# Optimization experiments

Measured on AMD Instinct MI355X. Metric: run time of the kernel, lower is better.

## Reference

```python
import jax, jax.numpy as jnp
import numpy as np

ALPHA = 0.2  # tf.nn.leaky_relu default

def leaky(x):
    return jnp.where(x >= 0, x, ALPHA * x)

def segment_softmax(score, seg, num_segments):
    m = jax.ops.segment_max(score, seg, num_segments=num_segments)
    e = jnp.exp(score - m[seg])
    denom = jax.ops.segment_sum(e, seg, num_segments=num_segments)
    return e / denom[seg]

def setup_inputs() -> dict:
    key = jax.random.key(0)
    ks = jax.random.split(key, 8)
    E, NE, NR, D, U = 500000, 100000, 1000, 128, 128
    return {
        "h_index": jax.random.randint(ks[0], (E,), 0, NE),
        "r_index": jax.random.randint(ks[1], (E,), 0, NR),
        "t_index": jax.random.randint(ks[2], (E,), 0, NE),
        "entity_embeddings": jax.random.normal(ks[3], (NE, D), jnp.float32),
        "relation_embeddings": jax.random.normal(ks[4], (NR, D), jnp.float32),
        "W": jax.random.normal(ks[5], (3 * D, U), jnp.float32) * 0.05,
        "a": jax.random.normal(ks[6], (U, 1), jnp.float32) * 0.1,
        "a_b": jnp.zeros((1,), jnp.float32),
        "bias": jnp.zeros((U,), jnp.float32),
    }

def reference(h_index, r_index, t_index, entity_embeddings, relation_embeddings, W, a, a_b, bias):
    num_entities = entity_embeddings.shape[0]
    h = entity_embeddings[h_index]          # [E, D]
    r = relation_embeddings[r_index]        # [E, D]
    t = entity_embeddings[t_index]          # [E, D]
    feats = jnp.concatenate([h, r, t], axis=-1) @ W  # [E, U]
    # att_kernel Dense(1, activation=leaky_relu), then wrapped again in att_activation
    score = leaky(leaky(feats @ a + a_b))[:, 0]      # [E]
    alpha = segment_softmax(score, h_index, num_entities)
    msg = feats * alpha[:, None]                     # gcn_mapper: edge features * weight
    reduced = jax.ops.segment_sum(msg, h_index, num_segments=num_entities)  # [NE, U]
    out = reduced + bias                             # identity_updater returns reduced_msg
    return jax.nn.relu(out)
```

## Files before the change

kernel.cpp:

```cpp
#include <hip/hip_runtime.h>
#include <hip/hip_bf16.h>

#define ALPHA2 0.04f

typedef __attribute__((ext_vector_type(8))) short short8;
typedef __attribute__((ext_vector_type(4))) float floatx4;
typedef __attribute__((ext_vector_type(8))) unsigned short ushort8;

__device__ __forceinline__ unsigned short f2bf(float f) {
    unsigned u = __float_as_uint(f);
    unsigned r = (u + 0x7fffu + ((u >> 16) & 1u)) >> 16;
    return (unsigned short)r;
}
__device__ __forceinline__ float bf2f(unsigned short h) {
    return __uint_as_float((unsigned)h << 16);
}

__device__ __forceinline__ void async_copy16(const float* g, float* lds_base) {
    __builtin_amdgcn_global_load_lds(
        (const __attribute__((address_space(1))) unsigned int*)g,
        (__attribute__((address_space(3))) unsigned int*)lds_base, 16, 0, 0);
}


__global__ void k_prep(const float* __restrict__ W, unsigned short* __restrict__ Bfr,
                       int* __restrict__ count, int NE) {
    int idx = blockIdx.x * blockDim.x + threadIdx.x;
    if (idx < 3 * 128 * 128) {
        int kk = idx & 7, n = (idx >> 3) & 127, g = idx >> 10;
        int slice = g >> 4, kc = (g >> 2) & 3, quad = g & 3;
        int k = kc * 32 + quad * 8 + kk;
        Bfr[idx] = f2bf(W[(size_t)(slice * 128 + k) * 128 + n]);
    }
    if (idx < NE) count[idx] = 0;
}

__global__ __launch_bounds__(256, 4) void k_gemm_all(
        const float* __restrict__ ent, const float* __restrict__ rel,
        const unsigned short* __restrict__ Bfr,
        unsigned short* __restrict__ Pb, unsigned short* __restrict__ Qb,
        unsigned short* __restrict__ Rb,
        float* __restrict__ s1, float* __restrict__ s3, float* __restrict__ s2,
        const float* __restrict__ avec, int NE, int NR, int NBent, int NBrel,
        const int* __restrict__ hidx, int* __restrict__ count,
        int* __restrict__ rank, int E) {
    __shared__ __align__(16) float Ash[64 * 128];
    int tid = threadIdx.x;
    int b = blockIdx.x;
    int ngemm = NBent + NBrel;

    if (b >= ngemm) {
        int e = (b - ngemm) * 256 + tid;
        if (e < E) rank[e] = atomicAdd(count + hidx[e], 1);
        return;
    }

    bool isEnt = b < NBent;
    const float* In = isEnt ? ent : rel;
    int nrows = isEnt ? NE : NR;
    int rowbase = (isEnt ? b : b - NBent) * 64;

    int wave = tid >> 6, lane = tid & 63;

    #pragma unroll
    for (int i = 0; i < 8; ++i) {
        int r = wave * 16 + i * 2 + (lane >> 5);
        int grow = rowbase + r;
        if (grow > nrows - 1) grow = nrows - 1;
        int c = (lane & 31) ^ (r & 7);
        async_copy16(In + (size_t)grow * 128 + c * 4,
                     Ash + (size_t)(wave * 16 + i * 2) * 128);
    }
    __syncthreads();

    int m16 = lane & 15, quad = lane >> 4;
    int rs = wave * 16;
    int R = rs + m16, sw = R & 7;
    const float4* rowp = (const float4*)(Ash + (size_t)R * 128);

    float av[8];
    #pragma unroll
    for (int j = 0; j < 8; ++j) av[j] = avec[j * 16 + m16];

    int nphase = isEnt ? 2 : 1;
    for (int ph = 0; ph < nphase; ++ph) {
        int slice; unsigned short* Out; float* svec;
        if (isEnt) { slice = ph ? 2 : 0; Out = ph ? Qb : Pb; svec = ph ? s3 : s1; }
        else       { slice = 1; Out = Rb; svec = s2; }

        floatx4 acc[8];
        #pragma unroll
        for (int j = 0; j < 8; ++j) acc[j] = (floatx4){0.f, 0.f, 0.f, 0.f};

        short8 bf0[8], bf1[8];
        auto loadB = [&](int kc, short8* dst) {
            const unsigned short* bb =
                Bfr + (size_t)((slice * 4 + kc) * 4 + quad) * 1024 + m16 * 8;
            #pragma unroll
            for (int j = 0; j < 8; ++j) dst[j] = *(const short8*)(bb + j * 128);
        };
        auto doMfma = [&](int kc, short8* bf) {
            int c0 = kc * 8 + quad * 2;
            float4 fa = rowp[c0 ^ sw];
            float4 fb = rowp[(c0 + 1) ^ sw];
            short8 af;
            af[0] = (short)f2bf(fa.x); af[1] = (short)f2bf(fa.y);
            af[2] = (short)f2bf(fa.z); af[3] = (short)f2bf(fa.w);
            af[4] = (short)f2bf(fb.x); af[5] = (short)f2bf(fb.y);
            af[6] = (short)f2bf(fb.z); af[7] = (short)f2bf(fb.w);
            #pragma unroll
            for (int j = 0; j < 8; ++j)
                acc[j] = __builtin_amdgcn_mfma_f32_16x16x32_bf16(af, bf[j], acc[j], 0, 0, 0);
        };
        loadB(0, bf0);
        loadB(1, bf1);
        doMfma(0, bf0);
        loadB(2, bf0);
        doMfma(1, bf1);
        loadB(3, bf1);
        doMfma(2, bf0);
        doMfma(3, bf1);

        #pragma unroll
        for (int reg = 0; reg < 4; ++reg) {
            int row = rowbase + rs + quad * 4 + reg;
            float part = 0.f;
            ushort8 v;
            #pragma unroll
            for (int j = 0; j < 8; ++j) {
                float x = acc[j][reg];
                part = fmaf(x, av[j], part);
                v[j] = f2bf(x);
            }
            #pragma unroll
            for (int off = 1; off < 16; off <<= 1) part += __shfl_xor(part, off);
            if (row < nrows) {
                *(ushort8*)(Out + (size_t)row * 128 + m16 * 8) = v;
                if (m16 == 0) svec[row] = part;
            }
        }
    }
}

__device__ __forceinline__ int block_incl_scan256(int s, int* sh, int t) {
    sh[t] = s; __syncthreads();
    #pragma unroll
    for (int off = 1; off < 256; off <<= 1) {
        int x = 0;
        if (t >= off) x = sh[t - off];
        __syncthreads();
        sh[t] += x;
        __syncthreads();
    }
    return sh[t];
}

__global__ __launch_bounds__(256) void k_scan_a(const int* __restrict__ count, int NE,
                                                int* __restrict__ bsum) {
    __shared__ int sh[256];
    int b = blockIdx.x, t = threadIdx.x;
    int base = b * 1024 + t * 4, s = 0;
    #pragma unroll
    for (int j = 0; j < 4; ++j) { int i = base + j; if (i < NE) s += count[i]; }
    sh[t] = s; __syncthreads();
    for (int off = 128; off > 0; off >>= 1) {
        if (t < off) sh[t] += sh[t + off];
        __syncthreads();
    }
    if (t == 0) bsum[b] = sh[0];
}

__global__ __launch_bounds__(256) void k_scan_c(const int* __restrict__ count, int NE,
                                                const int* __restrict__ bsum, int NB,
                                                int* __restrict__ rowstart, int E) {
    __shared__ int sh[256];
    int b = blockIdx.x, t = threadIdx.x;
    int sb = (t < NB) ? bsum[t] : 0;
    (void)block_incl_scan256(sb, sh, t);
    int base0 = (b == 0) ? 0 : sh[b - 1];
    __syncthreads();
    int base = b * 1024 + t * 4;
    int v[4]; int s = 0;
    #pragma unroll
    for (int j = 0; j < 4; ++j) { int i = base + j; v[j] = (i < NE) ? count[i] : 0; s += v[j]; }
    int incl = block_incl_scan256(s, sh, t);
    int excl = base0 + incl - s;
    #pragma unroll
    for (int j = 0; j < 4; ++j) {
        int i = base + j;
        if (i < NE) { rowstart[i] = excl; excl += v[j]; }
    }
    if (b == 0 && t == 0) rowstart[NE] = E;
}

__global__ void k_score_scatter(const int* __restrict__ h, const int* __restrict__ r,
                                const int* __restrict__ t, const float* __restrict__ s1,
                                const float* __restrict__ s2, const float* __restrict__ s3,
                                const float* __restrict__ a_b,
                                const int* __restrict__ rowstart, const int* __restrict__ rank,
                                uint2* __restrict__ rt_s, int E) {
    int e = blockIdx.x * blockDim.x + threadIdx.x;
    if (e >= E) return;
    int hi = h[e], ri = r[e], ti = t[e];
    float x = s1[hi] + s2[ri] + s3[ti] + a_b[0];
    float sc = (x >= 0.f) ? x : ALPHA2 * x;
    float ev = __expf(sc);
    rt_s[rowstart[hi] + rank[e]] = make_uint2(((unsigned)ri << 17) | (unsigned)ti,
                                              __float_as_uint(ev));
}

__global__ __launch_bounds__(256) void k_aggregate(const int* __restrict__ rowstart,
                                                   const uint2* __restrict__ rt_s,
                                                   const unsigned short* __restrict__ Pb,
                                                   const unsigned short* __restrict__ Qb,
                                                   const unsigned short* __restrict__ Rb,
                                                   const float* __restrict__ bias,
                                                   float* __restrict__ out, int NE) {
    int gid = blockIdx.x * blockDim.x + threadIdx.x;
    int n = gid >> 4;
    int sl = gid & 15;
    if (n >= NE) return;
    int start = rowstart[n], end = rowstart[n + 1];
    int c0 = sl * 8;
    float acc[8] = {};
    float evsum = 0.f;
    int i = start;
    for (; i + 4 <= end; i += 4) {
        uint2 m0 = rt_s[i], m1 = rt_s[i + 1], m2 = rt_s[i + 2], m3 = rt_s[i + 3];
        float ev0 = __uint_as_float(m0.y), ev1 = __uint_as_float(m1.y);
        float ev2 = __uint_as_float(m2.y), ev3 = __uint_as_float(m3.y);
        ushort8 q0 = *(const ushort8*)(Qb + (size_t)(m0.x & 0x1FFFFu) * 128 + c0);
        ushort8 rr0 = *(const ushort8*)(Rb + (size_t)(m0.x >> 17) * 128 + c0);
        ushort8 q1 = *(const ushort8*)(Qb + (size_t)(m1.x & 0x1FFFFu) * 128 + c0);
        ushort8 rr1 = *(const ushort8*)(Rb + (size_t)(m1.x >> 17) * 128 + c0);
        ushort8 q2 = *(const ushort8*)(Qb + (size_t)(m2.x & 0x1FFFFu) * 128 + c0);
        ushort8 rr2 = *(const ushort8*)(Rb + (size_t)(m2.x >> 17) * 128 + c0);
        ushort8 q3 = *(const ushort8*)(Qb + (size_t)(m3.x & 0x1FFFFu) * 128 + c0);
        ushort8 rr3 = *(const ushort8*)(Rb + (size_t)(m3.x >> 17) * 128 + c0);
        evsum += (ev0 + ev1) + (ev2 + ev3);
        #pragma unroll
        for (int j = 0; j < 8; ++j) {
            acc[j] = fmaf(ev0, bf2f(q0[j]) + bf2f(rr0[j]), acc[j]);
            acc[j] = fmaf(ev1, bf2f(q1[j]) + bf2f(rr1[j]), acc[j]);
            acc[j] = fmaf(ev2, bf2f(q2[j]) + bf2f(rr2[j]), acc[j]);
            acc[j] = fmaf(ev3, bf2f(q3[j]) + bf2f(rr3[j]), acc[j]);
        }
    }
    for (; i < end; ++i) {
        uint2 m0 = rt_s[i];
        float ev0 = __uint_as_float(m0.y);
        ushort8 q0 = *(const ushort8*)(Qb + (size_t)(m0.x & 0x1FFFFu) * 128 + c0);
        ushort8 rr0 = *(const ushort8*)(Rb + (size_t)(m0.x >> 17) * 128 + c0);
        evsum += ev0;
        #pragma unroll
        for (int j = 0; j < 8; ++j)
            acc[j] = fmaf(ev0, bf2f(q0[j]) + bf2f(rr0[j]), acc[j]);
    }
    float bi[8];
    #pragma unroll
    for (int j = 0; j < 8; ++j) bi[j] = bias[j * 16 + sl];
    float o[8];
    if (end > start) {
        float inv = 1.f / evsum;
        ushort8 pb = *(const ushort8*)(Pb + (size_t)n * 128 + c0);
        #pragma unroll
        for (int j = 0; j < 8; ++j) o[j] = bf2f(pb[j]) + acc[j] * inv + bi[j];
    } else {
        #pragma unroll
        for (int j = 0; j < 8; ++j) o[j] = bi[j];
    }
    #pragma unroll
    for (int j = 0; j < 8; ++j)
        out[(size_t)n * 128 + j * 16 + sl] = fmaxf(o[j], 0.f);
}

static inline size_t align_up(size_t x, size_t a) { return (x + a - 1) / a * a; }

extern "C" void kernel_launch(void* const* d_in, const int* in_sizes, int n_in,
                              void* d_out, int out_size, void* d_ws, size_t ws_size,
                              hipStream_t stream) {
    const int* h_index = (const int*)d_in[0];
    const int* r_index = (const int*)d_in[1];
    const int* t_index = (const int*)d_in[2];
    const float* ent = (const float*)d_in[3];
    const float* rel = (const float*)d_in[4];
    const float* W = (const float*)d_in[5];
    const float* a = (const float*)d_in[6];
    const float* a_b = (const float*)d_in[7];
    const float* bias = (const float*)d_in[8];
    float* out = (float*)d_out;

    int E = in_sizes[0];
    int NE = in_sizes[3] / 128;
    int NR = in_sizes[4] / 128;

    char* p = (char*)d_ws;
    auto alloc = [&](size_t bytes) { char* q = p; p += align_up(bytes, 256); return (void*)q; };
    unsigned short* Pb = (unsigned short*)alloc((size_t)NE * 128 * 2);
    unsigned short* Qb = (unsigned short*)alloc((size_t)NE * 128 * 2);
    unsigned short* Rb = (unsigned short*)alloc((size_t)NR * 128 * 2);
    unsigned short* Bfr = (unsigned short*)alloc((size_t)3 * 128 * 128 * 2);
    float* s1 = (float*)alloc((size_t)NE * 4);
    float* s3 = (float*)alloc((size_t)NE * 4);
    float* s2 = (float*)alloc((size_t)NR * 4);
    int* count = (int*)alloc((size_t)NE * 4);
    int* rowstart = (int*)alloc((size_t)(NE + 1) * 4);
    int* rank = (int*)alloc((size_t)E * 4);
    int NB = (NE + 1023) / 1024;
    int* bsum = (int*)alloc((size_t)NB * 4);
    uint2* rt_s = (uint2*)alloc((size_t)E * 8);
    (void)ws_size; (void)n_in; (void)out_size;

    int nprep = (NE > 3 * 128 * 128) ? NE : 3 * 128 * 128;
    k_prep<<<(nprep + 255) / 256, 256, 0, stream>>>(W, Bfr, count, NE);
    int NBent = (NE + 63) / 64, NBrel = (NR + 63) / 64;
    int NBcnt = (E + 255) / 256;
    k_gemm_all<<<NBent + NBrel + NBcnt, 256, 0, stream>>>(
        ent, rel, Bfr, Pb, Qb, Rb, s1, s3, s2, a, NE, NR, NBent, NBrel,
        h_index, count, rank, E);
    k_scan_a<<<NB, 256, 0, stream>>>(count, NE, bsum);
    k_scan_c<<<NB, 256, 0, stream>>>(count, NE, bsum, NB, rowstart, E);
    k_score_scatter<<<(E + 255) / 256, 256, 0, stream>>>(h_index, r_index, t_index,
                                                         s1, s2, s3, a_b, rowstart,
                                                         rank, rt_s, E);
    k_aggregate<<<(NE * 16 + 255) / 256, 256, 0, stream>>>(rowstart, rt_s, Pb, Qb, Rb,
                                                           bias, out, NE);
}
```

Measured before the change: 200.3 us.

## Fuse scan, score scatter and aggregation into one cooperative persistent kernel

Replaces the four post-GEMM launches (two scan passes, score scatter, aggregate) with a single cooperative kernel that uses grid-wide syncs between phases and grid-stride loops over edges and nodes. The aim is to remove kernel launch gaps and tail effects between small dependent kernels. It adds grid.sync costs, caps the grid at resident occupancy, and keeps the old multi-kernel path as a fallback if the cooperative launch fails.

```diff
diff --git a/kernel.cpp b/kernel.cpp
--- a/kernel.cpp
+++ b/kernel.cpp
@@ -1,5 +1,8 @@
 #include <hip/hip_runtime.h>
 #include <hip/hip_bf16.h>
+#include <hip/hip_cooperative_groups.h>
+
+namespace cg = cooperative_groups;
 
 #define ALPHA2 0.04f
 
@@ -155,71 +158,25 @@
     return sh[t];
 }
 
-__global__ __launch_bounds__(256) void k_scan_a(const int* __restrict__ count, int NE,
-                                                int* __restrict__ bsum) {
-    __shared__ int sh[256];
-    int b = blockIdx.x, t = threadIdx.x;
-    int base = b * 1024 + t * 4, s = 0;
-    #pragma unroll
-    for (int j = 0; j < 4; ++j) { int i = base + j; if (i < NE) s += count[i]; }
-    sh[t] = s; __syncthreads();
-    for (int off = 128; off > 0; off >>= 1) {
-        if (t < off) sh[t] += sh[t + off];
-        __syncthreads();
-    }
-    if (t == 0) bsum[b] = sh[0];
-}
-
-__global__ __launch_bounds__(256) void k_scan_c(const int* __restrict__ count, int NE,
-                                                const int* __restrict__ bsum, int NB,
-                                                int* __restrict__ rowstart, int E) {
-    __shared__ int sh[256];
-    int b = blockIdx.x, t = threadIdx.x;
-    int sb = (t < NB) ? bsum[t] : 0;
-    (void)block_incl_scan256(sb, sh, t);
-    int base0 = (b == 0) ? 0 : sh[b - 1];
-    __syncthreads();
-    int base = b * 1024 + t * 4;
-    int v[4]; int s = 0;
-    #pragma unroll
-    for (int j = 0; j < 4; ++j) { int i = base + j; v[j] = (i < NE) ? count[i] : 0; s += v[j]; }
-    int incl = block_incl_scan256(s, sh, t);
-    int excl = base0 + incl - s;
-    #pragma unroll
-    for (int j = 0; j < 4; ++j) {
-        int i = base + j;
-        if (i < NE) { rowstart[i] = excl; excl += v[j]; }
-    }
-    if (b == 0 && t == 0) rowstart[NE] = E;
-}
-
-__global__ void k_score_scatter(const int* __restrict__ h, const int* __restrict__ r,
-                                const int* __restrict__ t, const float* __restrict__ s1,
-                                const float* __restrict__ s2, const float* __restrict__ s3,
-                                const float* __restrict__ a_b,
-                                const int* __restrict__ rowstart, const int* __restrict__ rank,
-                                uint2* __restrict__ rt_s, int E) {
-    int e = blockIdx.x * blockDim.x + threadIdx.x;
-    if (e >= E) return;
+__device__ __forceinline__ void scatter_one(int e,
+        const int* __restrict__ h, const int* __restrict__ r, const int* __restrict__ t,
+        const float* __restrict__ s1, const float* __restrict__ s2,
+        const float* __restrict__ s3, float ab0,
+        const int* __restrict__ rowstart, const int* __restrict__ rank,
+        uint2* __restrict__ rt_s) {
     int hi = h[e], ri = r[e], ti = t[e];
-    float x = s1[hi] + s2[ri] + s3[ti] + a_b[0];
+    float x = s1[hi] + s2[ri] + s3[ti] + ab0;
     float sc = (x >= 0.f) ? x : ALPHA2 * x;
     float ev = __expf(sc);
     rt_s[rowstart[hi] + rank[e]] = make_uint2(((unsigned)ri << 17) | (unsigned)ti,
                                               __float_as_uint(ev));
 }
 
-__global__ __launch_bounds__(256) void k_aggregate(const int* __restrict__ rowstart,
-                                                   const uint2* __restrict__ rt_s,
-                                                   const unsigned short* __restrict__ Pb,
-                                                   const unsigned short* __restrict__ Qb,
-                                                   const unsigned short* __restrict__ Rb,
-                                                   const float* __restrict__ bias,
-                                                   float* __restrict__ out, int NE) {
-    int gid = blockIdx.x * blockDim.x + threadIdx.x;
-    int n = gid >> 4;
-    int sl = gid & 15;
-    if (n >= NE) return;
+__device__ __forceinline__ void agg_one(int n, int sl,
+        const int* __restrict__ rowstart, const uint2* __restrict__ rt_s,
+        const unsigned short* __restrict__ Pb, const unsigned short* __restrict__ Qb,
+        const unsigned short* __restrict__ Rb,
+        const float* __restrict__ bias, float* __restrict__ out) {
     int start = rowstart[n], end = rowstart[n + 1];
     int c0 = sl * 8;
     float acc[8] = {};
@@ -274,6 +231,123 @@
         out[(size_t)n * 128 + j * 16 + sl] = fmaxf(o[j], 0.f);
 }
 
+__global__ __launch_bounds__(256, 4) void k_post(
+        const int* __restrict__ count, int NE, int NB98,
+        int* __restrict__ bsum, int* __restrict__ rowstart, int E,
+        const int* __restrict__ h, const int* __restrict__ r, const int* __restrict__ t,
+        const float* __restrict__ s1, const float* __restrict__ s2,
+        const float* __restrict__ s3, const float* __restrict__ a_b,
+        const int* __restrict__ rank, uint2* __restrict__ rt_s,
+        const unsigned short* __restrict__ Pb, const unsigned short* __restrict__ Qb,
+        const unsigned short* __restrict__ Rb,
+        const float* __restrict__ bias, float* __restrict__ out) {
+    cg::grid_group grid = cg::this_grid();
+    __shared__ int sh[256];
+    int b = blockIdx.x, tx = threadIdx.x, nb = gridDim.x;
+
+    if (b < NB98) {
+        int base = b * 1024 + tx * 4, s = 0;
+        #pragma unroll
+        for (int j = 0; j < 4; ++j) { int i = base + j; if (i < NE) s += count[i]; }
+        sh[tx] = s; __syncthreads();
+        for (int off = 128; off > 0; off >>= 1) {
+            if (tx < off) sh[tx] += sh[tx + off];
+            __syncthreads();
+        }
+        if (tx == 0) bsum[b] = sh[0];
+    }
+    grid.sync();
+
+    if (b < NB98) {
+        int sb = (tx < NB98) ? bsum[tx] : 0;
+        (void)block_incl_scan256(sb, sh, tx);
+        int base0 = (b == 0) ? 0 : sh[b - 1];
+        __syncthreads();
+        int base = b * 1024 + tx * 4;
+        int v[4]; int s = 0;
+        #pragma unroll
+        for (int j = 0; j < 4; ++j) { int i = base + j; v[j] = (i < NE) ? count[i] : 0; s += v[j]; }
+        int incl = block_incl_scan256(s, sh, tx);
+        int excl = base0 + incl - s;
+        #pragma unroll
+        for (int j = 0; j < 4; ++j) {
+            int i = base + j;
+            if (i < NE) { rowstart[i] = excl; excl += v[j]; }
+        }
+        if (b == 0 && tx == 0) rowstart[NE] = E;
+    }
+    grid.sync();
+
+    float ab0 = a_b[0];
+    for (int e = b * 256 + tx; e < E; e += nb * 256)
+        scatter_one(e, h, r, t, s1, s2, s3, ab0, rowstart, rank, rt_s);
+    grid.sync();
+
+    int total = NE * 16;
+    for (int gid = b * 256 + tx; gid < total; gid += nb * 256)
+        agg_one(gid >> 4, gid & 15, rowstart, rt_s, Pb, Qb, Rb, bias, out);
+}
+
+__global__ __launch_bounds__(256) void k_scan_a(const int* __restrict__ count, int NE,
+                                                int* __restrict__ bsum) {
+    __shared__ int sh[256];
+    int b = blockIdx.x, t = threadIdx.x;
+    int base = b * 1024 + t * 4, s = 0;
+    #pragma unroll
+    for (int j = 0; j < 4; ++j) { int i = base + j; if (i < NE) s += count[i]; }
+    sh[t] = s; __syncthreads();
+    for (int off = 128; off > 0; off >>= 1) {
+        if (t < off) sh[t] += sh[t + off];
+        __syncthreads();
+    }
+    if (t == 0) bsum[b] = sh[0];
+}
+
+__global__ __launch_bounds__(256) void k_scan_c(const int* __restrict__ count, int NE,
+                                                const int* __restrict__ bsum, int NB,
+                                                int* __restrict__ rowstart, int E) {
+    __shared__ int sh[256];
+    int b = blockIdx.x, t = threadIdx.x;
+    int sb = (t < NB) ? bsum[t] : 0;
+    (void)block_incl_scan256(sb, sh, t);
+    int base0 = (b == 0) ? 0 : sh[b - 1];
+    __syncthreads();
+    int base = b * 1024 + t * 4;
+    int v[4]; int s = 0;
+    #pragma unroll
+    for (int j = 0; j < 4; ++j) { int i = base + j; v[j] = (i < NE) ? count[i] : 0; s += v[j]; }
+    int incl = block_incl_scan256(s, sh, t);
+    int excl = base0 + incl - s;
+    #pragma unroll
+    for (int j = 0; j < 4; ++j) {
+        int i = base + j;
+        if (i < NE) { rowstart[i] = excl; excl += v[j]; }
+    }
+    if (b == 0 && t == 0) rowstart[NE] = E;
+}
+
+__global__ void k_score_scatter(const int* __restrict__ h, const int* __restrict__ r,
+                                const int* __restrict__ t, const float* __restrict__ s1,
+                                const float* __restrict__ s2, const float* __restrict__ s3,
+                                const float* __restrict__ a_b,
+                                const int* __restrict__ rowstart, const int* __restrict__ rank,
+                                uint2* __restrict__ rt_s, int E) {
+    int e = blockIdx.x * blockDim.x + threadIdx.x;
+    if (e < E) scatter_one(e, h, r, t, s1, s2, s3, a_b[0], rowstart, rank, rt_s);
+}
+
+__global__ __launch_bounds__(256) void k_aggregate(const int* __restrict__ rowstart,
+                                                   const uint2* __restrict__ rt_s,
+                                                   const unsigned short* __restrict__ Pb,
+                                                   const unsigned short* __restrict__ Qb,
+                                                   const unsigned short* __restrict__ Rb,
+                                                   const float* __restrict__ bias,
+                                                   float* __restrict__ out, int NE) {
+    int gid = blockIdx.x * blockDim.x + threadIdx.x;
+    if ((gid >> 4) < NE)
+        agg_one(gid >> 4, gid & 15, rowstart, rt_s, Pb, Qb, Rb, bias, out);
+}
+
 static inline size_t align_up(size_t x, size_t a) { return (x + a - 1) / a * a; }
 
 extern "C" void kernel_launch(void* const* d_in, const int* in_sizes, int n_in,
@@ -318,11 +392,42 @@
     k_gemm_all<<<NBent + NBrel + NBcnt, 256, 0, stream>>>(
         ent, rel, Bfr, Pb, Qb, Rb, s1, s3, s2, a, NE, NR, NBent, NBrel,
         h_index, count, rank, E);
-    k_scan_a<<<NB, 256, 0, stream>>>(count, NE, bsum);
-    k_scan_c<<<NB, 256, 0, stream>>>(count, NE, bsum, NB, rowstart, E);
-    k_score_scatter<<<(E + 255) / 256, 256, 0, stream>>>(h_index, r_index, t_index,
-                                                         s1, s2, s3, a_b, rowstart,
-                                                         rank, rt_s, E);
-    k_aggregate<<<(NE * 16 + 255) / 256, 256, 0, stream>>>(rowstart, rt_s, Pb, Qb, Rb,
-                                                           bias, out, NE);
-}
+
+    static int blocksPerCU = 0;
+    static int numCU = 0;
+    if (blocksPerCU == 0) {
+        int dev = 0; hipGetDevice(&dev);
+        hipDeviceProp_t prop;
+        hipGetDeviceProperties(&prop, dev);
+        numCU = prop.multiProcessorCount;
+        int nbk = 0;
+        hipOccupancyMaxActiveBlocksPerMultiprocessor(&nbk, (const void*)k_post, 256, 0);
+        if (nbk < 1) nbk = 1;
+        if (nbk > 8) nbk = 8;
+        blocksPerCU = nbk;
+        if (numCU < 1) numCU = 256;
+    }
+    int gridPost = numCU * blocksPerCU;
+
+    void* kargs[] = {
+        (void*)&count, (void*)&NE, (void*)&NB,
+        (void*)&bsum, (void*)&rowstart, (void*)&E,
+        (void*)&h_index, (void*)&r_index, (void*)&t_index,
+        (void*)&s1, (void*)&s2, (void*)&s3, (void*)&a_b,
+        (void*)&rank, (void*)&rt_s,
+        (void*)&Pb, (void*)&Qb, (void*)&Rb,
+        (void*)&bias, (void*)&out
+    };
+    hipError_t ce = hipLaunchCooperativeKernel((const void*)k_post, dim3(gridPost),
+                                               dim3(256), kargs, 0, stream);
+    if (ce != hipSuccess) {
+        (void)hipGetLastError();
+        k_scan_a<<<NB, 256, 0, stream>>>(count, NE, bsum);
+        k_scan_c<<<NB, 256, 0, stream>>>(count, NE, bsum, NB, rowstart, E);
+        k_score_scatter<<<(E + 255) / 256, 256, 0, stream>>>(h_index, r_index, t_index,
+                                                             s1, s2, s3, a_b, rowstart,
+                                                             rank, rt_s, E);
+        k_aggregate<<<(NE * 16 + 255) / 256, 256, 0, stream>>>(rowstart, rt_s, Pb, Qb, Rb,
+                                                               bias, out, NE);
+    }
+}
```

Result: slower. 415.0 us (+107.3%).

## Move edge score computation into aggregate and shrink CSR payload to one word

Applied to the files above, without the earlier changes.

Score and exp computation moves out of the scatter kernel into the aggregation kernel. The CSR edge record shrinks from 8 to 4 bytes, since only packed relation and tail indices are stored. Each of the 16 lanes per node now recomputes the same exp from s2/s3 gathers, adding redundant loads and transcendental work in the aggregate loop. The count/rank blocks are also reordered to come first in the combined GEMM launch, so they get scheduled earlier.

```diff
diff --git a/kernel.cpp b/kernel.cpp
--- a/kernel.cpp
+++ b/kernel.cpp
@@ -41,24 +41,24 @@
         unsigned short* __restrict__ Pb, unsigned short* __restrict__ Qb,
         unsigned short* __restrict__ Rb,
         float* __restrict__ s1, float* __restrict__ s3, float* __restrict__ s2,
-        const float* __restrict__ avec, int NE, int NR, int NBent, int NBrel,
+        const float* __restrict__ avec, int NE, int NR, int NBcnt, int NBent,
         const int* __restrict__ hidx, int* __restrict__ count,
         int* __restrict__ rank, int E) {
     __shared__ __align__(16) float Ash[64 * 128];
     int tid = threadIdx.x;
     int b = blockIdx.x;
-    int ngemm = NBent + NBrel;
-
-    if (b >= ngemm) {
-        int e = (b - ngemm) * 256 + tid;
+
+    if (b < NBcnt) {
+        int e = b * 256 + tid;
         if (e < E) rank[e] = atomicAdd(count + hidx[e], 1);
         return;
     }
-
-    bool isEnt = b < NBent;
+    int gb = b - NBcnt;
+
+    bool isEnt = gb < NBent;
     const float* In = isEnt ? ent : rel;
     int nrows = isEnt ? NE : NR;
-    int rowbase = (isEnt ? b : b - NBent) * 64;
+    int rowbase = (isEnt ? gb : gb - NBent) * 64;
 
     int wave = tid >> 6, lane = tid & 63;
 
@@ -193,27 +193,25 @@
     if (b == 0 && t == 0) rowstart[NE] = E;
 }
 
-__global__ void k_score_scatter(const int* __restrict__ h, const int* __restrict__ r,
-                                const int* __restrict__ t, const float* __restrict__ s1,
-                                const float* __restrict__ s2, const float* __restrict__ s3,
-                                const float* __restrict__ a_b,
-                                const int* __restrict__ rowstart, const int* __restrict__ rank,
-                                uint2* __restrict__ rt_s, int E) {
+__global__ void k_scatter_rt(const int* __restrict__ h, const int* __restrict__ r,
+                             const int* __restrict__ t,
+                             const int* __restrict__ rowstart,
+                             const int* __restrict__ rank,
+                             unsigned* __restrict__ rt, int E) {
     int e = blockIdx.x * blockDim.x + threadIdx.x;
     if (e >= E) return;
-    int hi = h[e], ri = r[e], ti = t[e];
-    float x = s1[hi] + s2[ri] + s3[ti] + a_b[0];
-    float sc = (x >= 0.f) ? x : ALPHA2 * x;
-    float ev = __expf(sc);
-    rt_s[rowstart[hi] + rank[e]] = make_uint2(((unsigned)ri << 17) | (unsigned)ti,
-                                              __float_as_uint(ev));
+    rt[rowstart[h[e]] + rank[e]] = ((unsigned)r[e] << 17) | (unsigned)t[e];
 }
 
 __global__ __launch_bounds__(256) void k_aggregate(const int* __restrict__ rowstart,
-                                                   const uint2* __restrict__ rt_s,
+                                                   const unsigned* __restrict__ rt,
                                                    const unsigned short* __restrict__ Pb,
                                                    const unsigned short* __restrict__ Qb,
                                                    const unsigned short* __restrict__ Rb,
+                                                   const float* __restrict__ s1,
+                                                   const float* __restrict__ s2,
+                                                   const float* __restrict__ s3,
+                                                   const float* __restrict__ a_b,
                                                    const float* __restrict__ bias,
                                                    float* __restrict__ out, int NE) {
     int gid = blockIdx.x * blockDim.x + threadIdx.x;
@@ -222,21 +220,34 @@
     if (n >= NE) return;
     int start = rowstart[n], end = rowstart[n + 1];
     int c0 = sl * 8;
+    float base = s1[n] + a_b[0];
     float acc[8] = {};
     float evsum = 0.f;
     int i = start;
     for (; i + 4 <= end; i += 4) {
-        uint2 m0 = rt_s[i], m1 = rt_s[i + 1], m2 = rt_s[i + 2], m3 = rt_s[i + 3];
-        float ev0 = __uint_as_float(m0.y), ev1 = __uint_as_float(m1.y);
-        float ev2 = __uint_as_float(m2.y), ev3 = __uint_as_float(m3.y);
-        ushort8 q0 = *(const ushort8*)(Qb + (size_t)(m0.x & 0x1FFFFu) * 128 + c0);
-        ushort8 rr0 = *(const ushort8*)(Rb + (size_t)(m0.x >> 17) * 128 + c0);
-        ushort8 q1 = *(const ushort8*)(Qb + (size_t)(m1.x & 0x1FFFFu) * 128 + c0);
-        ushort8 rr1 = *(const ushort8*)(Rb + (size_t)(m1.x >> 17) * 128 + c0);
-        ushort8 q2 = *(const ushort8*)(Qb + (size_t)(m2.x & 0x1FFFFu) * 128 + c0);
-        ushort8 rr2 = *(const ushort8*)(Rb + (size_t)(m2.x >> 17) * 128 + c0);
-        ushort8 q3 = *(const ushort8*)(Qb + (size_t)(m3.x & 0x1FFFFu) * 128 + c0);
-        ushort8 rr3 = *(const ushort8*)(Rb + (size_t)(m3.x >> 17) * 128 + c0);
+        unsigned u0 = rt[i], u1 = rt[i + 1], u2 = rt[i + 2], u3 = rt[i + 3];
+        unsigned t0 = u0 & 0x1FFFFu, r0i = u0 >> 17;
+        unsigned t1 = u1 & 0x1FFFFu, r1i = u1 >> 17;
+        unsigned t2 = u2 & 0x1FFFFu, r2i = u2 >> 17;
+        unsigned t3 = u3 & 0x1FFFFu, r3i = u3 >> 17;
+        ushort8 q0 = *(const ushort8*)(Qb + (size_t)t0 * 128 + c0);
+        ushort8 rr0 = *(const ushort8*)(Rb + (size_t)r0i * 128 + c0);
+        ushort8 q1 = *(const ushort8*)(Qb + (size_t)t1 * 128 + c0);
+        ushort8 rr1 = *(const ushort8*)(Rb + (size_t)r1i * 128 + c0);
+        ushort8 q2 = *(const ushort8*)(Qb + (size_t)t2 * 128 + c0);
+        ushort8 rr2 = *(const ushort8*)(Rb + (size_t)r2i * 128 + c0);
+        ushort8 q3 = *(const ushort8*)(Qb + (size_t)t3 * 128 + c0);
+        ushort8 rr3 = *(const ushort8*)(Rb + (size_t)r3i * 128 + c0);
+        float x0 = base + s2[r0i] + s3[t0];
+        float x1 = base + s2[r1i] + s3[t1];
+        float x2 = base + s2[r2i] + s3[t2];
+        float x3 = base + s2[r3i] + s3[t3];
+        x0 = (x0 >= 0.f) ? x0 : ALPHA2 * x0;
+        x1 = (x1 >= 0.f) ? x1 : ALPHA2 * x1;
+        x2 = (x2 >= 0.f) ? x2 : ALPHA2 * x2;
+        x3 = (x3 >= 0.f) ? x3 : ALPHA2 * x3;
+        float ev0 = __expf(x0), ev1 = __expf(x1);
+        float ev2 = __expf(x2), ev3 = __expf(x3);
         evsum += (ev0 + ev1) + (ev2 + ev3);
         #pragma unroll
         for (int j = 0; j < 8; ++j) {
@@ -247,10 +258,13 @@
         }
     }
     for (; i < end; ++i) {
-        uint2 m0 = rt_s[i];
-        float ev0 = __uint_as_float(m0.y);
-        ushort8 q0 = *(const ushort8*)(Qb + (size_t)(m0.x & 0x1FFFFu) * 128 + c0);
-        ushort8 rr0 = *(const ushort8*)(Rb + (size_t)(m0.x >> 17) * 128 + c0);
+        unsigned u0 = rt[i];
+        unsigned t0 = u0 & 0x1FFFFu, r0i = u0 >> 17;
+        ushort8 q0 = *(const ushort8*)(Qb + (size_t)t0 * 128 + c0);
+        ushort8 rr0 = *(const ushort8*)(Rb + (size_t)r0i * 128 + c0);
+        float x0 = base + s2[r0i] + s3[t0];
+        x0 = (x0 >= 0.f) ? x0 : ALPHA2 * x0;
+        float ev0 = __expf(x0);
         evsum += ev0;
         #pragma unroll
         for (int j = 0; j < 8; ++j)
@@ -308,21 +322,21 @@
     int* rank = (int*)alloc((size_t)E * 4);
     int NB = (NE + 1023) / 1024;
     int* bsum = (int*)alloc((size_t)NB * 4);
-    uint2* rt_s = (uint2*)alloc((size_t)E * 8);
+    unsigned* rt = (unsigned*)alloc((size_t)E * 4);
     (void)ws_size; (void)n_in; (void)out_size;
 
     int nprep = (NE > 3 * 128 * 128) ? NE : 3 * 128 * 128;
     k_prep<<<(nprep + 255) / 256, 256, 0, stream>>>(W, Bfr, count, NE);
     int NBent = (NE + 63) / 64, NBrel = (NR + 63) / 64;
     int NBcnt = (E + 255) / 256;
-    k_gemm_all<<<NBent + NBrel + NBcnt, 256, 0, stream>>>(
-        ent, rel, Bfr, Pb, Qb, Rb, s1, s3, s2, a, NE, NR, NBent, NBrel,
+    k_gemm_all<<<NBcnt + NBent + NBrel, 256, 0, stream>>>(
+        ent, rel, Bfr, Pb, Qb, Rb, s1, s3, s2, a, NE, NR, NBcnt, NBent,
         h_index, count, rank, E);
     k_scan_a<<<NB, 256, 0, stream>>>(count, NE, bsum);
     k_scan_c<<<NB, 256, 0, stream>>>(count, NE, bsum, NB, rowstart, E);
-    k_score_scatter<<<(E + 255) / 256, 256, 0, stream>>>(h_index, r_index, t_index,
-                                                         s1, s2, s3, a_b, rowstart,
-                                                         rank, rt_s, E);
-    k_aggregate<<<(NE * 16 + 255) / 256, 256, 0, stream>>>(rowstart, rt_s, Pb, Qb, Rb,
-                                                           bias, out, NE);
-}
+    k_scatter_rt<<<(E + 255) / 256, 256, 0, stream>>>(h_index, r_index, t_index,
+                                                      rowstart, rank, rt, E);
+    k_aggregate<<<(NE * 16 + 255) / 256, 256, 0, stream>>>(rowstart, rt, Pb, Qb, Rb,
+                                                           s1, s2, s3, a_b, bias,
+                                                           out, NE);
+}
```

After: 202.8 us. Within noise of the previous version (+1.3%).
